# Kernel tuning notes

Hardware: AMD Instinct MI355X
Metric: run time of the kernel (lower is better)

## Reference

```python
import jax, jax.numpy as jnp
import numpy as np

B, S, D, H = 4, 2048, 1024, 16
DK = D // H  # 64


def setup_inputs() -> dict:
    key = jax.random.key(0)
    ks = jax.random.split(key, 5)
    scale = 1.0 / np.sqrt(D)
    return {
        "embeddings": jax.random.normal(ks[0], (B, S, D), dtype=jnp.float32),
        "W_q": jax.random.normal(ks[1], (D, D), dtype=jnp.float32) * scale,
        "W_k": jax.random.normal(ks[2], (D, D), dtype=jnp.float32) * scale,
        "W_v": jax.random.normal(ks[3], (D, D), dtype=jnp.float32) * scale,
        "W_o": jax.random.normal(ks[4], (D, D), dtype=jnp.float32) * scale,
    }


def reference(embeddings, W_q, W_k, W_v, W_o):
    # torch nn.Linear: y = x @ W.T  (weights are [out, in])
    b, s, d = embeddings.shape
    h, dk = H, DK
    q = embeddings @ W_q.T  # [b, s, d]
    k = embeddings @ W_k.T
    v = embeddings @ W_v.T
    # split heads along last dim (matches the per-head slicing in the torch loop)
    q = q.reshape(b, s, h, dk)
    k = k.reshape(b, s, h, dk)
    v = v.reshape(b, s, h, dk)
    scores = jnp.einsum("bqhd,bkhd->bhqk", q, k) / jnp.sqrt(jnp.float32(dk))
    p = jax.nn.softmax(scores, axis=-1)  # dropout is identity at eval
    ctx = jnp.einsum("bhqk,bkhd->bqhd", p, v).reshape(b, s, d)
    return ctx @ W_o.T
```

## Files before the change

kernel.cpp:

```cpp
#include <hip/hip_runtime.h>
#include <hip/hip_bf16.h>

typedef unsigned short u16;
typedef __attribute__((ext_vector_type(8))) short bf16x8;
typedef __attribute__((ext_vector_type(4))) float f32x4;
typedef __attribute__((ext_vector_type(2))) unsigned int u32x2;

#define AS1 __attribute__((address_space(1)))
#define AS3 __attribute__((address_space(3)))

constexpr int Bc = 4, Sc = 2048, Dc = 1024, Hc = 16, DKc = 64;
constexpr size_t EDc = (size_t)Bc * Sc * Dc;
constexpr size_t WDc = (size_t)Dc * Dc;

__device__ __forceinline__ void g2l16(const void* g, void* l) {
  __builtin_amdgcn_global_load_lds((const AS1 unsigned int*)g,
                                   (AS3 unsigned int*)l, 16, 0, 0);
}

__device__ __forceinline__ u16 f2b(float f) {
  union { float f; unsigned u; } x; x.f = f;
  unsigned r = x.u + 0x7fffu + ((x.u >> 16) & 1u);
  return (u16)(r >> 16);
}

#if __has_builtin(__builtin_amdgcn_cvt_pk_bf16_f32)
typedef __attribute__((ext_vector_type(2))) __bf16 hbf2;
__device__ __forceinline__ unsigned f2b_pk(float a, float b) {
  union { hbf2 v; unsigned u; } x;
  x.v = __builtin_amdgcn_cvt_pk_bf16_f32(a, b);
  return x.u;
}
#else
__device__ __forceinline__ unsigned f2b_pk(float a, float b) {
  return (unsigned)f2b(a) | ((unsigned)f2b(b) << 16);
}
#endif

__device__ __forceinline__ float fast_exp2(float x) {
#if __has_builtin(__builtin_amdgcn_exp2f)
  return __builtin_amdgcn_exp2f(x);
#else
  return exp2f(x);
#endif
}

__global__ __launch_bounds__(256)
void cvt_all(const float* __restrict__ e, const float* __restrict__ wq,
             const float* __restrict__ wk, const float* __restrict__ wv,
             const float* __restrict__ wo, u16* __restrict__ dst) {
  int bx = blockIdx.x;
  const float* src;
  size_t doff;
  int chunk;
  if (bx < 4096) {
    src = e; doff = 0; chunk = bx;
  } else {
    int t = bx - 4096;
    int w = t >> 9;
    chunk = t & 511;
    src = (w == 0) ? wq : (w == 1) ? wk : (w == 2) ? wv : wo;
    doff = EDc + (size_t)w * WDc;
  }
  size_t i = ((size_t)chunk * 256 + threadIdx.x) * 8;
  float4 a = *(const float4*)(src + i);
  float4 b = *(const float4*)(src + i + 4);
  bf16x8 o;
  o[0] = (short)f2b(a.x); o[1] = (short)f2b(a.y);
  o[2] = (short)f2b(a.z); o[3] = (short)f2b(a.w);
  o[4] = (short)f2b(b.x); o[5] = (short)f2b(b.y);
  o[6] = (short)f2b(b.z); o[7] = (short)f2b(b.w);
  *(bf16x8*)(dst + doff + i) = o;
}

__global__ __launch_bounds__(256, 2)
void gemm_qkv(const u16* __restrict__ X, const u16* __restrict__ Wq,
              const u16* __restrict__ Wk, const u16* __restrict__ Wv,
              u16* __restrict__ Qo, u16* __restrict__ Ko,
              u16* __restrict__ VTo) {
  constexpr int BM = 128, BK = 64, K = Dc, N = Dc;
  __shared__ u16 As[BM * BK];
  __shared__ u16 Bs[BM * BK];

  const int tid = threadIdx.x;
  const int wave = tid >> 6, lane = tid & 63;
  const int mr = lane & 15, quad = lane >> 4, mr7 = lane & 7;
  const int sect = blockIdx.x >> 3;
  const int n0 = (blockIdx.x & 7) * 128;
  const int m0 = blockIdx.y * BM;
  const u16* W = (sect == 0) ? Wq : (sect == 1) ? Wk : Wv;
  const int wm = (wave >> 1) * 64, wn = (wave & 1) * 64;
  const int ldr = lane >> 3;
  const int ldc_sw = ((lane & 7) ^ (ldr & 7)) * 8;
  const bool vsec = (sect == 2);

  const f32x4 zero = {0.f, 0.f, 0.f, 0.f};
  f32x4 acc[4][4];
  #pragma unroll
  for (int i = 0; i < 4; i++)
    #pragma unroll
    for (int j = 0; j < 4; j++) acc[i][j] = zero;

  for (int k0 = 0; k0 < K; k0 += BK) {
    __syncthreads();
    #pragma unroll
    for (int i = 0; i < 4; i++) {
      int row = wave * 32 + i * 8;
      g2l16(X + (size_t)(m0 + row + ldr) * K + k0 + ldc_sw, As + row * BK);
      g2l16(W + (size_t)(n0 + row + ldr) * K + k0 + ldc_sw, Bs + row * BK);
    }
    __syncthreads();

    #pragma unroll
    for (int c = 0; c < 2; c++) {
      bf16x8 a[4], b[4];
      #pragma unroll
      for (int i = 0; i < 4; i++)
        a[i] = *(const bf16x8*)(As + (wm + i * 16 + mr) * BK +
                                (((c * 4 + quad) ^ mr7) * 8));
      #pragma unroll
      for (int j = 0; j < 4; j++)
        b[j] = *(const bf16x8*)(Bs + (wn + j * 16 + mr) * BK +
                                (((c * 4 + quad) ^ mr7) * 8));
      if (vsec) {
        #pragma unroll
        for (int i = 0; i < 4; i++)
          #pragma unroll
          for (int j = 0; j < 4; j++)
            acc[i][j] = __builtin_amdgcn_mfma_f32_16x16x32_bf16(
                b[j], a[i], acc[i][j], 0, 0, 0);
      } else {
        #pragma unroll
        for (int i = 0; i < 4; i++)
          #pragma unroll
          for (int j = 0; j < 4; j++)
            acc[i][j] = __builtin_amdgcn_mfma_f32_16x16x32_bf16(
                a[i], b[j], acc[i][j], 0, 0, 0);
      }
    }
  }

  if (vsec) {
    #pragma unroll
    for (int i = 0; i < 4; i++) {
      int s_glob = m0 + wm + i * 16 + mr;
      int bb = s_glob >> 11, s = s_glob & 2047;
      #pragma unroll
      for (int j = 0; j < 4; j++) {
        int nbase = n0 + wn + j * 16 + quad * 4;
        #pragma unroll
        for (int r = 0; r < 4; r++) {
          int n = nbase + r;
          int h = n >> 6, d = n & 63;
          VTo[((size_t)((bb * Hc + h) * DKc + d)) * Sc + s] = f2b(acc[i][j][r]);
        }
      }
    }
  } else {
    const float scale = (sect == 0) ? 0.18033688f : 1.0f;
    u16* Y = (sect == 0) ? Qo : Ko;
    #pragma unroll
    for (int i = 0; i < 4; i++)
      #pragma unroll
      for (int j = 0; j < 4; j++)
        #pragma unroll
        for (int r = 0; r < 4; r++) {
          int m = m0 + wm + i * 16 + quad * 4 + r;
          int n = n0 + wn + j * 16 + mr;
          Y[(size_t)m * N + n] = f2b(acc[i][j][r] * scale);
        }
  }
}

__global__ __launch_bounds__(256, 2)
void gemm_out(const u16* __restrict__ X, const u16* __restrict__ W,
              float* __restrict__ Y, int M, int N, int K) {
  constexpr int BM = 128, BK = 64;
  __shared__ u16 As[BM * BK];
  __shared__ u16 Bs[BM * BK];

  const int tid = threadIdx.x;
  const int wave = tid >> 6, lane = tid & 63;
  const int mr = lane & 15, quad = lane >> 4, mr7 = lane & 7;
  const int m0 = blockIdx.y * BM, n0 = blockIdx.x * BM;
  const int wm = (wave >> 1) * 64, wn = (wave & 1) * 64;
  const int ldr = lane >> 3;
  const int ldc_sw = ((lane & 7) ^ (ldr & 7)) * 8;

  const f32x4 zero = {0.f, 0.f, 0.f, 0.f};
  f32x4 acc[4][4];
  #pragma unroll
  for (int i = 0; i < 4; i++)
    #pragma unroll
    for (int j = 0; j < 4; j++) acc[i][j] = zero;

  for (int k0 = 0; k0 < K; k0 += BK) {
    __syncthreads();
    #pragma unroll
    for (int i = 0; i < 4; i++) {
      int row = wave * 32 + i * 8;
      g2l16(X + (size_t)(m0 + row + ldr) * K + k0 + ldc_sw, As + row * BK);
      g2l16(W + (size_t)(n0 + row + ldr) * K + k0 + ldc_sw, Bs + row * BK);
    }
    __syncthreads();

    #pragma unroll
    for (int c = 0; c < 2; c++) {
      bf16x8 a[4], b[4];
      #pragma unroll
      for (int i = 0; i < 4; i++)
        a[i] = *(const bf16x8*)(As + (wm + i * 16 + mr) * BK +
                                (((c * 4 + quad) ^ mr7) * 8));
      #pragma unroll
      for (int j = 0; j < 4; j++)
        b[j] = *(const bf16x8*)(Bs + (wn + j * 16 + mr) * BK +
                                (((c * 4 + quad) ^ mr7) * 8));
      #pragma unroll
      for (int i = 0; i < 4; i++)
        #pragma unroll
        for (int j = 0; j < 4; j++)
          acc[i][j] = __builtin_amdgcn_mfma_f32_16x16x32_bf16(
              a[i], b[j], acc[i][j], 0, 0, 0);
    }
  }

  #pragma unroll
  for (int i = 0; i < 4; i++)
    #pragma unroll
    for (int j = 0; j < 4; j++)
      #pragma unroll
      for (int r = 0; r < 4; r++) {
        int m = m0 + wm + i * 16 + quad * 4 + r;
        int n = n0 + wn + j * 16 + mr;
        Y[(size_t)m * N + n] = acc[i][j][r];
      }
}

__global__ __launch_bounds__(256, 4)
void attn(const u16* __restrict__ Q, const u16* __restrict__ K,
          const u16* __restrict__ VT, u16* __restrict__ O) {
  __shared__ u16 Ks[2][64 * 64];
  __shared__ u16 Vs[2][64 * 64];
  __shared__ u16 Ps[4][16 * 64];

  const int tid = threadIdx.x;
  const int wave = tid >> 6, lane = tid & 63;
  const int mr = lane & 15, quad = lane >> 4, mr7 = lane & 7;
  const int bh = blockIdx.y;
  const int b = bh >> 4, h = bh & 15;
  const int q0 = blockIdx.x * 128;
  const size_t headK = (size_t)b * Sc * Dc + (size_t)h * DKc;
  const size_t headV = (size_t)bh * DKc * Sc;
  const int ldr = lane >> 3;
  const int ldc_sw = ((lane & 7) ^ (ldr & 7)) * 8;

  const int row0a = wave * 16, row0b = wave * 16 + 8;
  const int pa_r = row0a + ldr, pb_r = row0b + ldr;
  const int sra = ((pa_r & 15) << 2) | (pa_r >> 4);
  const int srb = ((pb_r & 15) << 2) | (pb_r >> 4);

  bf16x8 qa[2][2];
  #pragma unroll
  for (int t = 0; t < 2; t++)
    #pragma unroll
    for (int c = 0; c < 2; c++)
      qa[t][c] = *(const bf16x8*)(Q + headK +
          (size_t)(q0 + wave * 32 + t * 16 + mr) * Dc + c * 32 + quad * 8);

  bf16x8 ones;
  #pragma unroll
  for (int j = 0; j < 8; j++) ones[j] = (short)0x3F80;

  const f32x4 zero = {0.f, 0.f, 0.f, 0.f};
  f32x4 o[2][4];
  f32x4 ol[2];
  #pragma unroll
  for (int t = 0; t < 2; t++) {
    ol[t] = zero;
    #pragma unroll
    for (int i = 0; i < 4; i++) o[t][i] = zero;
  }

  u16* Pw = Ps[wave];

  {
    const u16* Kb_ = K + headK;
    const u16* Vb_ = VT + headV;
    g2l16(Kb_ + (size_t)sra * Dc + ldc_sw, Ks[0] + row0a * 64);
    g2l16(Kb_ + (size_t)srb * Dc + ldc_sw, Ks[0] + row0b * 64);
    g2l16(Vb_ + (size_t)(row0a + ldr) * Sc + ldc_sw, Vs[0] + row0a * 64);
    g2l16(Vb_ + (size_t)(row0b + ldr) * Sc + ldc_sw, Vs[0] + row0b * 64);
  }
  __syncthreads();

  for (int kt = 0; kt < Sc / 64; kt++) {
    const int cur = kt & 1;
    if (kt + 1 < Sc / 64) {
      const int nk0 = (kt + 1) * 64;
      const int nxt = cur ^ 1;
      g2l16(K + headK + (size_t)(nk0 + sra) * Dc + ldc_sw, Ks[nxt] + row0a * 64);
      g2l16(K + headK + (size_t)(nk0 + srb) * Dc + ldc_sw, Ks[nxt] + row0b * 64);
      g2l16(VT + headV + (size_t)(row0a + ldr) * Sc + nk0 + ldc_sw, Vs[nxt] + row0a * 64);
      g2l16(VT + headV + (size_t)(row0b + ldr) * Sc + nk0 + ldc_sw, Vs[nxt] + row0b * 64);
    }

    f32x4 s0[4], s1[4];
    #pragma unroll
    for (int kc = 0; kc < 4; kc++) {
      s0[kc] = zero; s1[kc] = zero;
      #pragma unroll
      for (int c = 0; c < 2; c++) {
        bf16x8 kb = *(const bf16x8*)(Ks[cur] + (kc * 16 + mr) * 64 +
                                     (((c * 4 + quad) ^ mr7) * 8));
        s0[kc] = __builtin_amdgcn_mfma_f32_16x16x32_bf16(qa[0][c], kb, s0[kc], 0, 0, 0);
        s1[kc] = __builtin_amdgcn_mfma_f32_16x16x32_bf16(qa[1][c], kb, s1[kc], 0, 0, 0);
      }
    }

    bf16x8 pa[2][2];
    #pragma unroll
    for (int t = 0; t < 2; t++) {
      f32x4* s = t ? s1 : s0;
      #pragma unroll
      for (int r = 0; r < 4; r++) {
        float p0 = fast_exp2(s[0][r]);
        float p1 = fast_exp2(s[1][r]);
        float p2 = fast_exp2(s[2][r]);
        float p3 = fast_exp2(s[3][r]);
        u32x2 w;
        w.x = f2b_pk(p0, p1);
        w.y = f2b_pk(p2, p3);
        *(u32x2*)(Pw + (quad * 4 + r) * 64 + mr * 4) = w;
      }
      #pragma unroll
      for (int c = 0; c < 2; c++)
        pa[t][c] = *(const bf16x8*)(Pw + mr * 64 + c * 32 + quad * 8);
      #pragma unroll
      for (int c = 0; c < 2; c++)
        ol[t] = __builtin_amdgcn_mfma_f32_16x16x32_bf16(pa[t][c], ones, ol[t], 0, 0, 0);
    }

    #pragma unroll
    for (int ni = 0; ni < 4; ni++)
      #pragma unroll
      for (int c = 0; c < 2; c++) {
        bf16x8 vb = *(const bf16x8*)(Vs[cur] + (ni * 16 + mr) * 64 +
                                     (((c * 4 + quad) ^ mr7) * 8));
        o[0][ni] = __builtin_amdgcn_mfma_f32_16x16x32_bf16(pa[0][c], vb, o[0][ni], 0, 0, 0);
        o[1][ni] = __builtin_amdgcn_mfma_f32_16x16x32_bf16(pa[1][c], vb, o[1][ni], 0, 0, 0);
      }

    __syncthreads();
  }

  #pragma unroll
  for (int t = 0; t < 2; t++)
    #pragma unroll
    for (int r = 0; r < 4; r++) {
      float inv = 1.0f / ol[t][r];
      #pragma unroll
      for (int ni = 0; ni < 4; ni++) {
        int qq = q0 + wave * 32 + t * 16 + quad * 4 + r;
        O[headK + (size_t)qq * Dc + ni * 16 + mr] = f2b(o[t][ni][r] * inv);
      }
    }
}

extern "C" void kernel_launch(void* const* d_in, const int* in_sizes, int n_in,
                              void* d_out, int out_size, void* d_ws, size_t ws_size,
                              hipStream_t stream) {
  const float* emb = (const float*)d_in[0];
  const float* Wq  = (const float*)d_in[1];
  const float* Wk  = (const float*)d_in[2];
  const float* Wv  = (const float*)d_in[3];
  const float* Wo  = (const float*)d_in[4];
  float* out = (float*)d_out;

  const int M = Bc * Sc;

  u16* Eb  = (u16*)d_ws;
  u16* Wqb = Eb  + EDc;
  u16* Wkb = Wqb + WDc;
  u16* Wvb = Wkb + WDc;
  u16* Wob = Wvb + WDc;
  u16* Qb  = Wob + WDc;
  u16* Kb  = Qb  + EDc;
  u16* VTb = Kb  + EDc;
  u16* Cb  = Qb;

  dim3 blk(256);
  cvt_all<<<dim3(4096 + 4 * 512), blk, 0, stream>>>(emb, Wq, Wk, Wv, Wo, Eb);

  gemm_qkv<<<dim3(24, M / 128), blk, 0, stream>>>(Eb, Wqb, Wkb, Wvb,
                                                  Qb, Kb, VTb);

  attn<<<dim3(Sc / 128, Bc * Hc), blk, 0, stream>>>(Qb, Kb, VTb, Cb);

  gemm_out<<<dim3(Dc / 128, M / 128), blk, 0, stream>>>(Cb, Wob, out,
                                                        M, Dc, Dc);
}
```

Measured before the change: 274.6 us.

## Double attention query tile per block and compute row sums on VALU

Each attention block now handles 256 queries (64 per wave, four 16-row subtiles), so every K/V tile loaded into LDS is reused across twice as many queries and K/V fragments are read into registers once per tile. The row-sum MFMA against a ones vector is replaced by VALU accumulation of the fp32 probabilities, followed by a cross-lane shuffle reduction at the end. This costs more registers (launch bounds drop to 2 blocks per CU), a larger P scratch area in LDS, and half as many blocks in the grid.

```diff
diff --git a/kernel.cpp b/kernel.cpp
--- a/kernel.cpp
+++ b/kernel.cpp
@@ -236,19 +236,19 @@
       }
 }
 
-__global__ __launch_bounds__(256, 4)
+__global__ __launch_bounds__(256, 2)
 void attn(const u16* __restrict__ Q, const u16* __restrict__ K,
           const u16* __restrict__ VT, u16* __restrict__ O) {
   __shared__ u16 Ks[2][64 * 64];
   __shared__ u16 Vs[2][64 * 64];
-  __shared__ u16 Ps[4][16 * 64];
+  __shared__ u16 Ps[16][16 * 64];
 
   const int tid = threadIdx.x;
   const int wave = tid >> 6, lane = tid & 63;
   const int mr = lane & 15, quad = lane >> 4, mr7 = lane & 7;
   const int bh = blockIdx.y;
   const int b = bh >> 4, h = bh & 15;
-  const int q0 = blockIdx.x * 128;
+  const int q0 = blockIdx.x * 256;
   const size_t headK = (size_t)b * Sc * Dc + (size_t)h * DKc;
   const size_t headV = (size_t)bh * DKc * Sc;
   const int ldr = lane >> 3;
@@ -259,29 +259,24 @@
   const int sra = ((pa_r & 15) << 2) | (pa_r >> 4);
   const int srb = ((pb_r & 15) << 2) | (pb_r >> 4);
 
-  bf16x8 qa[2][2];
-  #pragma unroll
-  for (int t = 0; t < 2; t++)
+  bf16x8 qa[4][2];
+  #pragma unroll
+  for (int sub = 0; sub < 4; sub++)
     #pragma unroll
     for (int c = 0; c < 2; c++)
-      qa[t][c] = *(const bf16x8*)(Q + headK +
-          (size_t)(q0 + wave * 32 + t * 16 + mr) * Dc + c * 32 + quad * 8);
-
-  bf16x8 ones;
-  #pragma unroll
-  for (int j = 0; j < 8; j++) ones[j] = (short)0x3F80;
+      qa[sub][c] = *(const bf16x8*)(Q + headK +
+          (size_t)(q0 + wave * 64 + sub * 16 + mr) * Dc + c * 32 + quad * 8);
 
   const f32x4 zero = {0.f, 0.f, 0.f, 0.f};
-  f32x4 o[2][4];
-  f32x4 ol[2];
-  #pragma unroll
-  for (int t = 0; t < 2; t++) {
-    ol[t] = zero;
-    #pragma unroll
-    for (int i = 0; i < 4; i++) o[t][i] = zero;
-  }
-
-  u16* Pw = Ps[wave];
+  f32x4 o[4][4];
+  float lrow[4][4];
+  #pragma unroll
+  for (int sub = 0; sub < 4; sub++)
+    #pragma unroll
+    for (int i = 0; i < 4; i++) {
+      o[sub][i] = zero;
+      lrow[sub][i] = 0.f;
+    }
 
   {
     const u16* Kb_ = K + headK;
@@ -304,64 +299,78 @@
       g2l16(VT + headV + (size_t)(row0b + ldr) * Sc + nk0 + ldc_sw, Vs[nxt] + row0b * 64);
     }
 
-    f32x4 s0[4], s1[4];
-    #pragma unroll
-    for (int kc = 0; kc < 4; kc++) {
-      s0[kc] = zero; s1[kc] = zero;
-      #pragma unroll
-      for (int c = 0; c < 2; c++) {
-        bf16x8 kb = *(const bf16x8*)(Ks[cur] + (kc * 16 + mr) * 64 +
+    bf16x8 kb[4][2];
+    #pragma unroll
+    for (int kc = 0; kc < 4; kc++)
+      #pragma unroll
+      for (int c = 0; c < 2; c++)
+        kb[kc][c] = *(const bf16x8*)(Ks[cur] + (kc * 16 + mr) * 64 +
                                      (((c * 4 + quad) ^ mr7) * 8));
-        s0[kc] = __builtin_amdgcn_mfma_f32_16x16x32_bf16(qa[0][c], kb, s0[kc], 0, 0, 0);
-        s1[kc] = __builtin_amdgcn_mfma_f32_16x16x32_bf16(qa[1][c], kb, s1[kc], 0, 0, 0);
-      }
-    }
-
-    bf16x8 pa[2][2];
-    #pragma unroll
-    for (int t = 0; t < 2; t++) {
-      f32x4* s = t ? s1 : s0;
+
+    #pragma unroll
+    for (int sub = 0; sub < 4; sub++) {
+      f32x4 s[4];
+      #pragma unroll
+      for (int kc = 0; kc < 4; kc++) {
+        s[kc] = zero;
+        #pragma unroll
+        for (int c = 0; c < 2; c++)
+          s[kc] = __builtin_amdgcn_mfma_f32_16x16x32_bf16(
+              qa[sub][c], kb[kc][c], s[kc], 0, 0, 0);
+      }
+      u16* Pw = Ps[wave * 4 + sub];
       #pragma unroll
       for (int r = 0; r < 4; r++) {
         float p0 = fast_exp2(s[0][r]);
         float p1 = fast_exp2(s[1][r]);
         float p2 = fast_exp2(s[2][r]);
         float p3 = fast_exp2(s[3][r]);
+        lrow[sub][r] += (p0 + p1) + (p2 + p3);
         u32x2 w;
         w.x = f2b_pk(p0, p1);
         w.y = f2b_pk(p2, p3);
         *(u32x2*)(Pw + (quad * 4 + r) * 64 + mr * 4) = w;
       }
+    }
+
+    bf16x8 vb[4][2];
+    #pragma unroll
+    for (int ni = 0; ni < 4; ni++)
       #pragma unroll
       for (int c = 0; c < 2; c++)
-        pa[t][c] = *(const bf16x8*)(Pw + mr * 64 + c * 32 + quad * 8);
-      #pragma unroll
-      for (int c = 0; c < 2; c++)
-        ol[t] = __builtin_amdgcn_mfma_f32_16x16x32_bf16(pa[t][c], ones, ol[t], 0, 0, 0);
-    }
-
-    #pragma unroll
-    for (int ni = 0; ni < 4; ni++)
-      #pragma unroll
-      for (int c = 0; c < 2; c++) {
-        bf16x8 vb = *(const bf16x8*)(Vs[cur] + (ni * 16 + mr) * 64 +
+        vb[ni][c] = *(const bf16x8*)(Vs[cur] + (ni * 16 + mr) * 64 +
                                      (((c * 4 + quad) ^ mr7) * 8));
-        o[0][ni] = __builtin_amdgcn_mfma_f32_16x16x32_bf16(pa[0][c], vb, o[0][ni], 0, 0, 0);
-        o[1][ni] = __builtin_amdgcn_mfma_f32_16x16x32_bf16(pa[1][c], vb, o[1][ni], 0, 0, 0);
-      }
+
+    #pragma unroll
+    for (int sub = 0; sub < 4; sub++) {
+      const u16* Pw = Ps[wave * 4 + sub];
+      bf16x8 pa0 = *(const bf16x8*)(Pw + mr * 64 + quad * 8);
+      bf16x8 pa1 = *(const bf16x8*)(Pw + mr * 64 + 32 + quad * 8);
+      #pragma unroll
+      for (int ni = 0; ni < 4; ni++) {
+        o[sub][ni] = __builtin_amdgcn_mfma_f32_16x16x32_bf16(
+            pa0, vb[ni][0], o[sub][ni], 0, 0, 0);
+        o[sub][ni] = __builtin_amdgcn_mfma_f32_16x16x32_bf16(
+            pa1, vb[ni][1], o[sub][ni], 0, 0, 0);
+      }
+    }
 
     __syncthreads();
   }
 
   #pragma unroll
-  for (int t = 0; t < 2; t++)
+  for (int sub = 0; sub < 4; sub++)
     #pragma unroll
     for (int r = 0; r < 4; r++) {
-      float inv = 1.0f / ol[t][r];
+      float l = lrow[sub][r];
+      #pragma unroll
+      for (int off = 1; off < 16; off <<= 1)
+        l += __shfl_xor(l, off, 64);
+      float inv = 1.0f / l;
       #pragma unroll
       for (int ni = 0; ni < 4; ni++) {
-        int qq = q0 + wave * 32 + t * 16 + quad * 4 + r;
-        O[headK + (size_t)qq * Dc + ni * 16 + mr] = f2b(o[t][ni][r] * inv);
+        int qq = q0 + wave * 64 + sub * 16 + quad * 4 + r;
+        O[headK + (size_t)qq * Dc + ni * 16 + mr] = f2b(o[sub][ni][r] * inv);
       }
     }
 }
@@ -394,7 +403,7 @@
   gemm_qkv<<<dim3(24, M / 128), blk, 0, stream>>>(Eb, Wqb, Wkb, Wvb,
                                                   Qb, Kb, VTb);
 
-  attn<<<dim3(Sc / 128, Bc * Hc), blk, 0, stream>>>(Qb, Kb, VTb, Cb);
+  attn<<<dim3(Sc / 256, Bc * Hc), blk, 0, stream>>>(Qb, Kb, VTb, Cb);
 
   gemm_out<<<dim3(Dc / 128, M / 128), blk, 0, stream>>>(Cb, Wob, out,
                                                         M, Dc, Dc);
```

Result: no change. 270.2 us (-1.6%).
